# Optimization experiments

Hardware: AMD Instinct MI355X
Metric: run time of the kernel (lower is better)

## Reference

```python
import jax, jax.numpy as jnp
import numpy as np

C = 64  # RDN out_dim

def _make_coord_1d(n):
    r = 1.0 / n
    return -1.0 + r + 2.0 * r * jnp.arange(n, dtype=jnp.float32)

def _unfold3x3(feat):
    # torch F.unfold(feat, 3, padding=1) -> [B, C*9, H, W], ordering c*9 + (ki*3+kj)
    B, Cc, H, W = feat.shape
    p = jnp.pad(feat, ((0, 0), (0, 0), (1, 1), (1, 1)))
    patches = jnp.stack([p[:, :, di:di + H, dj:dj + W]
                         for di in range(3) for dj in range(3)], axis=2)
    return patches.reshape(B, Cc * 9, H, W)

def setup_inputs() -> dict:
    key = jax.random.key(0)
    ks = jax.random.split(key, 5)
    feat = jax.random.normal(ks[0], (1, C, 64, 64), dtype=jnp.float32)
    w1 = jax.random.normal(ks[1], (3, 256), dtype=jnp.float32) * 0.1
    b1 = jax.random.normal(ks[2], (256,), dtype=jnp.float32) * 0.01
    w2 = jax.random.normal(ks[3], (256, C * 9 * 3), dtype=jnp.float32) * 0.02
    b2 = jax.random.normal(ks[4], (C * 9 * 3,), dtype=jnp.float32) * 0.01
    return {"feat": feat, "w1": w1, "b1": b1, "w2": w2, "b2": b2,
            "out_h": 256, "out_w": 256}

def reference(feat, w1, b1, w2, b2, out_h, out_w):
    B, Cc, H, W = feat.shape
    C9 = Cc * 9
    # HR query coords at grid centers, flattened: [q, 2] (dim0 -> H axis)
    cy = _make_coord_1d(out_h)
    cx = _make_coord_1d(out_w)
    coord = jnp.stack(jnp.meshgrid(cy, cx, indexing='ij'), axis=-1).reshape(-1, 2)
    coord = jnp.broadcast_to(coord[None], (B, out_h * out_w, 2))  # [B, q, 2]
    cell = jnp.stack([jnp.full((out_h * out_w,), 2.0 / out_h, jnp.float32),
                      jnp.full((out_h * out_w,), 2.0 / out_w, jnp.float32)], axis=-1)
    cell = jnp.broadcast_to(cell[None], (B, out_h * out_w, 2))

    featu = _unfold3x3(feat)  # [B, C*9, H, W]

    # coord_ = coord - cell/2, clamped query coords
    coord_ = coord - cell * 0.5
    eps = 1e-6
    coord_q = jnp.clip(coord_ + eps, -1.0 + eps, 1.0 - eps)

    # grid_sample nearest, align_corners=False: idx = round(((c+1)*N - 1)/2)
    iy = jnp.clip(jnp.round(((coord_q[..., 0] + 1.0) * H - 1.0) * 0.5), 0, H - 1).astype(jnp.int32)
    ix = jnp.clip(jnp.round(((coord_q[..., 1] + 1.0) * W - 1.0) * 0.5), 0, W - 1).astype(jnp.int32)

    # gather unfolded features at nearest LR cells -> [B, q, C*9]
    q_feat = jax.vmap(lambda f, y, x: f[:, y, x])(featu, iy, ix)  # [B, C9, q]
    q_feat = jnp.swapaxes(q_feat, 1, 2)

    # feat_coord (shifted by half a cell) at gathered indices = -1 + 2*i/N
    q_coord0 = -1.0 + 2.0 * iy.astype(jnp.float32) / H
    q_coord1 = -1.0 + 2.0 * ix.astype(jnp.float32) / W

    rel0 = (coord_[..., 0] - q_coord0) * (H * 0.5)
    rel1 = (coord_[..., 1] - q_coord1) * (W * 0.5)
    r_rev = cell[..., 0] * (H * 0.5)
    mlp_in = jnp.stack([rel0, rel1, r_rev], axis=-1)  # [B, q, 3]

    h = jax.nn.relu(jnp.einsum('bqi,ih->bqh', mlp_in, w1) + b1)
    pred_w = (jnp.einsum('bqh,ho->bqo', h, w2) + b2).reshape(B, -1, C9, 3)

    # per-query 1xC9 @ C9x3 bmm
    rgb = jnp.einsum('bqc,bqco->bqo', q_feat, pred_w)  # [B, q, 3]
    return rgb.reshape(B, out_h, out_w, 3).transpose(0, 3, 1, 2)
```

## Files before the change

### kernel.cpp

```cpp
#include <hip/hip_runtime.h>


#define NOUT 1728

typedef short bf16x8 __attribute__((ext_vector_type(8)));
typedef float f32x4  __attribute__((ext_vector_type(4)));

__device__ inline unsigned short bf16r(float a) {
    const unsigned ua = __builtin_bit_cast(unsigned, a);
    return (unsigned short)((ua + 0x7FFFu + ((ua >> 16) & 1u)) >> 16);
}
__device__ inline unsigned bf16pack(float a, float b) {
    unsigned ua = __builtin_bit_cast(unsigned, a);
    unsigned ub = __builtin_bit_cast(unsigned, b);
    ua = (ua + 0x7FFFu + ((ua >> 16) & 1u)) >> 16;
    ub = (ub + 0x7FFFu + ((ub >> 16) & 1u)) >> 16;
    return ua | (ub << 16);
}

__global__ __launch_bounds__(256) void k_prep(
    const float* __restrict__ w1, const float* __restrict__ b1,
    const float* __restrict__ w2, const float* __restrict__ b2,
    const float* __restrict__ feat,
    unsigned short* __restrict__ predw16, float* __restrict__ featT)
{
    __shared__ float h4[4][256];
    __shared__ float redA[1024];
    __shared__ float ftile[64][65];

    const int tid = threadIdx.x;
    const int bid = blockIdx.x;

    if (bid < 108) {
        const int sg    = bid / 27;
        const int chunk = bid - sg * 27;
        const int o_l   = tid & 63;
        const int q     = tid >> 6;
        const int o     = chunk * 64 + o_l;

        {
            const float wa = w1[tid];
            const float wb = w1[256 + tid];
            const float wc = w1[512 + tid];
            const float bb = b1[tid];
            #pragma unroll
            for (int si = 0; si < 4; ++si) {
                h4[si][tid] = fmaxf(
                    fmaf(wa, (float)sg * 0.25f,
                    fmaf(wb, (float)si * 0.25f,
                    fmaf(wc, 0.25f, bb))), 0.0f);
            }
        }
        __syncthreads();

        const float* w2c = w2 + (q << 6) * NOUT + o;
        const float* hq0 = &h4[0][q << 6];
        const float* hq1 = &h4[1][q << 6];
        const float* hq2 = &h4[2][q << 6];
        const float* hq3 = &h4[3][q << 6];

        float a0 = 0.f, a1 = 0.f, a2 = 0.f, a3 = 0.f;
        #pragma unroll 16
        for (int j = 0; j < 64; ++j) {
            const float v = w2c[j * NOUT];
            a0 = fmaf(hq0[j], v, a0);
            a1 = fmaf(hq1[j], v, a1);
            a2 = fmaf(hq2[j], v, a2);
            a3 = fmaf(hq3[j], v, a3);
        }
        *(float4*)&redA[tid << 2] = make_float4(a0, a1, a2, a3);
        __syncthreads();

        {
            const int ol = tid >> 2;
            const int si = tid & 3;
            const int oo = chunk * 64 + ol;
            float a = redA[(0 * 64 + ol) * 4 + si]
                    + redA[(1 * 64 + ol) * 4 + si]
                    + redA[(2 * 64 + ol) * 4 + si]
                    + redA[(3 * 64 + ol) * 4 + si] + b2[oo];
            const int ct = oo / 3;
            const int k  = oo - ct * 3;
            const int c  = (ct * 7282) >> 16;
            const int tp = ct - c * 9;
            const int m  = ((sg << 2) + si) * 3 + k;
            predw16[m * 576 + tp * 64 + c] = bf16r(a);
        }
    } else {
        const int y  = bid - 108;
        const int cq = tid >> 6;
        const int xl = tid & 63;
        #pragma unroll
        for (int p = 0; p < 16; ++p) {
            const int c = (p << 2) + cq;
            ftile[c][xl] = feat[c * 4096 + y * 64 + xl];
        }
        __syncthreads();
        float* dst = featT + y * 4096;
        #pragma unroll
        for (int p = 0; p < 16; ++p) {
            const int x = (p << 2) + cq;
            dst[x * 64 + xl] = ftile[xl][x];
        }
    }
}

__global__ __launch_bounds__(768, 1) void k_conv(
    const float* __restrict__ featT, const unsigned short* __restrict__ predw16,
    float* __restrict__ out)
{
    __shared__ f32x4 red[9 * 64];

    const int tid  = threadIdx.x;
    const int lane = tid & 63;
    const int wave = tid >> 6;
    const int mt   = wave >> 2;
    const int wv   = wave & 3;
    const int bid  = blockIdx.x;
    const int sx   = bid & 7;
    const int u    = bid >> 3;
    const int y0   = (sx << 3) | (u >> 2);
    const int x0   = (u & 3) << 4;

    const int lc = lane & 15;
    const int lk = lane >> 4;

    int xb[3]; float xmsk[3];
    #pragma unroll
    for (int d = 0; d < 3; ++d) {
        const int rx = x0 + lc + d - 1;
        xmsk[d] = ((unsigned)rx < 64u) ? 1.0f : 0.0f;
        xb[d] = (rx < 0 ? 0 : (rx > 63 ? 63 : rx)) << 6;
    }
    int yb[3]; float ymsk[3];
    #pragma unroll
    for (int d = 0; d < 3; ++d) {
        const int ry = y0 + d - 1;
        ymsk[d] = ((unsigned)ry < 64u) ? 1.0f : 0.0f;
        yb[d] = (ry < 0 ? 0 : (ry > 63 ? 63 : ry)) << 12;
    }

    const unsigned short* arow = predw16 + (mt * 16 + lc) * 576 + (lk << 3);

    f32x4 acc = {0.0f, 0.0f, 0.0f, 0.0f};

    #pragma unroll
    for (int i = 0; i < 5; ++i) {
        const int kk  = wv + (i << 2);
        const int kkc = kk > 17 ? 17 : kk;
        const float vld = (kk < 18) ? 1.0f : 0.0f;
        const int tap = kkc >> 1;
        const int dr  = (tap >= 6) ? 2 : (tap >= 3 ? 1 : 0);
        const int dc  = tap - dr * 3;
        const int c0  = ((kkc & 1) << 5) + (lk << 3);
        const float* fb = featT + yb[dr] + xb[dc] + c0;
        const float  mk = ymsk[dr] * xmsk[dc] * vld;

        const float4 fa = *(const float4*)fb;
        const float4 fc = *(const float4*)(fb + 4);

        uint4 bb;
        bb.x = bf16pack(fa.x * mk, fa.y * mk);
        bb.y = bf16pack(fa.z * mk, fa.w * mk);
        bb.z = bf16pack(fc.x * mk, fc.y * mk);
        bb.w = bf16pack(fc.z * mk, fc.w * mk);
        const bf16x8 bfrag = __builtin_bit_cast(bf16x8, bb);
        const bf16x8 afrag = *(const bf16x8*)(arow + 32 * kkc);

        acc = __builtin_amdgcn_mfma_f32_16x16x32_bf16(afrag, bfrag, acc,
                                                      0, 0, 0);
    }

    if (wv > 0) red[(mt * 3 + (wv - 1)) * 64 + lane] = acc;
    __syncthreads();

    if (wv == 0) {
        #pragma unroll
        for (int q = 0; q < 3; ++q) {
            const f32x4 pv = red[(mt * 3 + q) * 64 + lane];
            acc[0] += pv[0]; acc[1] += pv[1]; acc[2] += pv[2]; acc[3] += pv[3];
        }
        #pragma unroll
        for (int r = 0; r < 4; ++r) {
            const int m = mt * 16 + (lk << 2) + r;
            const int s = (m * 171) >> 9;
            const int k = m - s * 3;
            const int y = (y0 << 2) + (s >> 2);
            const int x = ((x0 + lc) << 2) + (s & 3);
            out[k * 65536 + y * 256 + x] = acc[r];
        }
    }
}

extern "C" void kernel_launch(void* const* d_in, const int* in_sizes, int n_in,
                              void* d_out, int out_size, void* d_ws, size_t ws_size,
                              hipStream_t stream) {
    const float* feat = (const float*)d_in[0];
    const float* w1   = (const float*)d_in[1];
    const float* b1   = (const float*)d_in[2];
    const float* w2   = (const float*)d_in[3];
    const float* b2   = (const float*)d_in[4];
    float* out = (float*)d_out;

    unsigned short* predw16 = (unsigned short*)d_ws;
    float* featT = (float*)((char*)d_ws + 57344);

    hipLaunchKernelGGL(k_prep, dim3(172), dim3(256), 0, stream,
                       w1, b1, w2, b2, feat, predw16, featT);
    hipLaunchKernelGGL(k_conv, dim3(256), dim3(768), 0, stream,
                       featT, predw16, out);
}
```

Measured before the change: 16.91 us.

## Split transpose and conv work into smaller, more numerous blocks

The feature transpose in the prep kernel now uses 256 blocks, each covering a 16-channel by 64-pixel tile with float4 stores, instead of 64 blocks each handling a full row of 64 channels. The conv kernel moves from 256 blocks of 768 threads (3 M-tiles per block) to 768 blocks of 256 threads with one M-tile each, shrinking the shared reduction buffer. The aim is to spread work across more CUs and cut per-block latency. In exchange, each block reloads the feature fragments separately per M-tile and more blocks must be scheduled.

```diff
diff --git a/kernel.cpp b/kernel.cpp
--- a/kernel.cpp
+++ b/kernel.cpp
@@ -26,7 +26,7 @@
 {
     __shared__ float h4[4][256];
     __shared__ float redA[1024];
-    __shared__ float ftile[64][65];
+    __shared__ float tile[16][65];
 
     const int tid = threadIdx.x;
     const int bid = blockIdx.x;
@@ -87,40 +87,45 @@
             predw16[m * 576 + tp * 64 + c] = bf16r(a);
         }
     } else {
-        const int y  = bid - 108;
-        const int cq = tid >> 6;
-        const int xl = tid & 63;
-        #pragma unroll
-        for (int p = 0; p < 16; ++p) {
-            const int c = (p << 2) + cq;
-            ftile[c][xl] = feat[c * 4096 + y * 64 + xl];
+        const int b  = bid - 108;
+        const int y  = b & 63;
+        const int cq = b >> 6;
+        {
+            const int cl = tid >> 6;
+            const int x  = tid & 63;
+            #pragma unroll
+            for (int p = 0; p < 4; ++p)
+                tile[p * 4 + cl][x] =
+                    feat[((cq << 4) + p * 4 + cl) * 4096 + (y << 6) + x];
         }
         __syncthreads();
-        float* dst = featT + y * 4096;
-        #pragma unroll
-        for (int p = 0; p < 16; ++p) {
-            const int x = (p << 2) + cq;
-            dst[x * 64 + xl] = ftile[xl][x];
-        }
-    }
-}
-
-__global__ __launch_bounds__(768, 1) void k_conv(
+        {
+            const int x  = tid >> 2;
+            const int c4 = (tid & 3) << 2;
+            float4 v;
+            v.x = tile[c4 + 0][x];
+            v.y = tile[c4 + 1][x];
+            v.z = tile[c4 + 2][x];
+            v.w = tile[c4 + 3][x];
+            *(float4*)&featT[(y << 12) + (x << 6) + (cq << 4) + c4] = v;
+        }
+    }
+}
+
+__global__ __launch_bounds__(256, 1) void k_conv(
     const float* __restrict__ featT, const unsigned short* __restrict__ predw16,
     float* __restrict__ out)
 {
-    __shared__ f32x4 red[9 * 64];
+    __shared__ f32x4 red[3 * 64];
 
     const int tid  = threadIdx.x;
     const int lane = tid & 63;
-    const int wave = tid >> 6;
-    const int mt   = wave >> 2;
-    const int wv   = wave & 3;
+    const int wv   = tid >> 6;
     const int bid  = blockIdx.x;
-    const int sx   = bid & 7;
-    const int u    = bid >> 3;
-    const int y0   = (sx << 3) | (u >> 2);
-    const int x0   = (u & 3) << 4;
+    const int mt   = bid >> 8;
+    const int nt   = bid & 255;
+    const int y0   = nt >> 2;
+    const int x0   = (nt & 3) << 4;
 
     const int lc = lane & 15;
     const int lk = lane >> 4;
@@ -171,13 +176,13 @@
                                                       0, 0, 0);
     }
 
-    if (wv > 0) red[(mt * 3 + (wv - 1)) * 64 + lane] = acc;
+    if (wv > 0) red[(wv - 1) * 64 + lane] = acc;
     __syncthreads();
 
     if (wv == 0) {
         #pragma unroll
         for (int q = 0; q < 3; ++q) {
-            const f32x4 pv = red[(mt * 3 + q) * 64 + lane];
+            const f32x4 pv = red[q * 64 + lane];
             acc[0] += pv[0]; acc[1] += pv[1]; acc[2] += pv[2]; acc[3] += pv[3];
         }
         #pragma unroll
@@ -205,8 +210,8 @@
     unsigned short* predw16 = (unsigned short*)d_ws;
     float* featT = (float*)((char*)d_ws + 57344);
 
-    hipLaunchKernelGGL(k_prep, dim3(172), dim3(256), 0, stream,
+    hipLaunchKernelGGL(k_prep, dim3(364), dim3(256), 0, stream,
                        w1, b1, w2, b2, feat, predw16, featT);
-    hipLaunchKernelGGL(k_conv, dim3(256), dim3(768), 0, stream,
+    hipLaunchKernelGGL(k_conv, dim3(768), dim3(256), 0, stream,
                        featT, predw16, out);
 }
```

New measurement: 16.82 us. No clear change (-0.5%).
